# Optimization experiments

Hardware: AMD Instinct MI355X
Metric: run time of the kernel (lower is better)

## Reference

```python
import jax, jax.numpy as jnp
import numpy as np

N = 20000      # nodes
E = 320000     # edges (before self-loops)
C_IN, C_HID, C_OUT = 256, 256, 128
NEG_SLOPE = 0.2  # PyG GATConv default


def setup_inputs() -> dict:
    key = jax.random.key(0)
    ks = jax.random.split(key, 10)
    x = jax.random.normal(ks[0], (N, C_IN), dtype=jnp.float32)
    edge_index = jax.random.randint(ks[1], (2, E), 0, N, dtype=jnp.int64)

    def glorot(k, shape, fan):
        return jax.random.normal(k, shape, dtype=jnp.float32) / np.float32(np.sqrt(fan))

    W1 = glorot(ks[2], (C_IN, C_HID), C_IN)
    a_src1 = glorot(ks[3], (C_HID,), C_HID)
    a_dst1 = glorot(ks[4], (C_HID,), C_HID)
    b1 = jnp.zeros((C_HID,), jnp.float32)
    W2 = glorot(ks[5], (C_HID, C_OUT), C_HID)
    a_src2 = glorot(ks[6], (C_OUT,), C_OUT)
    a_dst2 = glorot(ks[7], (C_OUT,), C_OUT)
    b2 = jnp.zeros((C_OUT,), jnp.float32)
    return dict(x=x, edge_index=edge_index, W1=W1, a_src1=a_src1, a_dst1=a_dst1,
                b1=b1, W2=W2, a_src2=a_src2, a_dst2=a_dst2, b2=b2)


def gat_layer(x, src, dst, W, a_src, a_dst, b, n):
    # PyG GATConv (heads=1): linear proj, additive attention, softmax over
    # incoming edges per destination node, weighted aggregation + bias.
    h = x @ W                                   # [N, F]
    alpha_src = h @ a_src                       # [N]
    alpha_dst = h @ a_dst                       # [N]
    e = jax.nn.leaky_relu(alpha_src[src] + alpha_dst[dst], NEG_SLOPE)  # [E]
    m = jax.ops.segment_max(e, dst, num_segments=n)                    # stable softmax
    e = jnp.exp(e - m[dst])
    denom = jax.ops.segment_sum(e, dst, num_segments=n)                # [N]
    out = jax.ops.segment_sum(e[:, None] * h[src], dst, num_segments=n)  # [N, F]
    return out / denom[:, None] + b


def reference(x, edge_index, W1, a_src1, a_dst1, b1, W2, a_src2, a_dst2, b2):
    n = x.shape[0]
    # GATConv adds self-loops by default
    loops = jnp.arange(n, dtype=edge_index.dtype)
    ei = jnp.concatenate([edge_index, jnp.stack([loops, loops])], axis=1)
    src, dst = ei[0], ei[1]
    h = gat_layer(x, src, dst, W1, a_src1, a_dst1, b1, n)
    h = jax.nn.relu(h)  # Dropout is identity in eval mode
    return gat_layer(h, src, dst, W2, a_src2, a_dst2, b2, n)
```

## Files before the change

### kernel.cpp

```cpp
#include <hip/hip_runtime.h>
#include <math.h>

#define N_NODES 20000
#define N_EDGES 320000
#define E_TOT   (N_EDGES + N_NODES)
#define C_IN  256
#define C_HID 256
#define C_OUT 128
#define NEG_SLOPE 0.2f
#define CAP   256

typedef __attribute__((ext_vector_type(8))) short bf16x8;
typedef __attribute__((ext_vector_type(4))) float f32x4;

__device__ __align__(16) unsigned short c_W1h[C_IN * C_HID], c_W1l[C_IN * C_HID];
__device__ __align__(16) unsigned short c_W2h[C_HID * C_OUT], c_W2l[C_HID * C_OUT];
__device__ float c_as1f[C_HID], c_ad1f[C_HID], c_b1f[C_HID];
__device__ float c_as2f[C_OUT], c_ad2f[C_OUT], c_b2f[C_OUT];
__device__ __align__(16) unsigned short g_h1b[(size_t)N_NODES * C_HID];
__device__ __align__(16) unsigned short g_g1h[(size_t)N_NODES * C_HID];
__device__ __align__(16) unsigned short g_g1l[(size_t)N_NODES * C_HID];
__device__ __align__(16) unsigned short g_h2b[(size_t)N_NODES * C_OUT];
__device__ float g_alps1[N_NODES], g_alpd1[N_NODES];
__device__ float g_alps2[N_NODES], g_alpd2[N_NODES];
__device__ int   g_cursor[N_NODES];
__device__ int   g_srcidx[(size_t)N_NODES * CAP];
__device__ int   g_is64;
__device__ int   g_isf32;

__device__ __forceinline__ float bf2f(unsigned short b){
  unsigned int u = ((unsigned int)b) << 16;
  return __builtin_bit_cast(float, u);
}
__device__ __forceinline__ unsigned short f2bf(float f){
  unsigned int u = __builtin_bit_cast(unsigned int, f);
  u += 0x7fffu + ((u >> 16) & 1u);
  return (unsigned short)(u >> 16);
}
__device__ __forceinline__ int clampi(int v){
  v = v < 0 ? 0 : v;
  return v >= N_NODES ? N_NODES - 1 : v;
}
__device__ __forceinline__ void edge_sd(const int* ei, int e, int& s, int& d){
  if (e < N_EDGES){
    if (g_is64){ s = ei[2 * e]; d = ei[2 * (N_EDGES + e)]; }
    else       { s = ei[e];     d = ei[N_EDGES + e]; }
    s = clampi(s); d = clampi(d);
  } else {
    s = d = e - N_EDGES;
  }
}

struct Ptrs { const void* p[8]; };

__device__ __forceinline__ int wpack(int k, int n, int Nc){
  return (((k >> 5) * (Nc / 16) + (n >> 4)) * 64 + (((k >> 3) & 3) * 16 + (n & 15))) * 8 + (k & 7);
}

#define PREP_Z  N_NODES
#define PREP_W1 (C_IN * C_HID)
#define PREP_W2 (C_HID * C_OUT)
#define PREP_T  (PREP_Z + PREP_W1 + PREP_W2 + 2 * C_HID + C_HID + 2 * C_OUT + C_OUT)

__global__ void prep_k(const unsigned int* __restrict__ xw,
                       const int* __restrict__ ei, Ptrs ps){
  __shared__ int s_isf32;
  if (threadIdx.x < 64){
    int lane = (int)threadIdx.x, cnt = 0;
    for (int j = lane; j < 256; j += 64){
      unsigned int e = (xw[j] >> 7) & 0xFFu;
      if (e >= 0x60u && e <= 0x8Fu) ++cnt;
    }
#pragma unroll
    for (int o = 32; o > 0; o >>= 1) cnt += __shfl_xor(cnt, o, 64);
    if (lane == 0) s_isf32 = (cnt < 200) ? 1 : 0;
  }
  __syncthreads();
  const int isf32 = s_isf32;

  if (blockIdx.x == 0 && threadIdx.x < 64){
    unsigned long long anybad = __ballot(ei[2 * (int)threadIdx.x + 1] != 0);
    if (threadIdx.x == 0){ g_isf32 = isf32; g_is64 = (anybad == 0ULL) ? 1 : 0; }
  }

  int tid = (int)(blockIdx.x * blockDim.x + threadIdx.x);
  if (tid < PREP_Z){
    g_cursor[tid] = 0;
    g_alps1[tid] = 0.f; g_alpd1[tid] = 0.f;
    g_alps2[tid] = 0.f; g_alpd2[tid] = 0.f;
    return;
  }
  int j = tid - PREP_Z;
  auto ld = [&](const void* p, int i) -> float {
    return isf32 ? ((const float*)p)[i] : bf2f(((const unsigned short*)p)[i]);
  };
  if (j < PREP_W1){
    float f = ld(ps.p[0], j);
    int k = j / C_HID, n = j % C_HID;
    int idx = wpack(k, n, C_HID);
    unsigned short h = f2bf(f);
    c_W1h[idx] = h; c_W1l[idx] = f2bf(f - bf2f(h));
    return;
  }
  j -= PREP_W1;
  if (j < PREP_W2){
    float f = ld(ps.p[4], j);
    int k = j / C_OUT, n = j % C_OUT;
    int idx = wpack(k, n, C_OUT);
    unsigned short h = f2bf(f);
    c_W2h[idx] = h; c_W2l[idx] = f2bf(f - bf2f(h));
    return;
  }
  j -= PREP_W2;
  if      (j <  256) c_as1f[j]        = ld(ps.p[1], j);
  else if (j <  512) c_ad1f[j - 256]  = ld(ps.p[2], j - 256);
  else if (j <  768) c_b1f [j - 512]  = ld(ps.p[3], j - 512);
  else if (j <  896) c_as2f[j - 768]  = ld(ps.p[5], j - 768);
  else if (j < 1024) c_ad2f[j - 896]  = ld(ps.p[6], j - 896);
  else if (j < 1152) c_b2f [j - 1024] = ld(ps.p[7], j - 1024);
}

__global__ void scatter_k(const int* __restrict__ ei){
  int e = blockIdx.x * blockDim.x + threadIdx.x;
  if (e >= E_TOT) return;
  int s, d;
  edge_sd(ei, e, s, d);
  int pos = atomicAdd(&g_cursor[d], 1);
  if (pos < CAP) g_srcidx[(size_t)d * CAP + pos] = s;
}

template<int SEL>
__global__ __launch_bounds__(256) void gemm_k(const void* __restrict__ xsrc){
  const int Nc = SEL ? C_OUT : C_HID;
  const int NT = SEL ? 2 : 4;
  const unsigned short* Wh = SEL ? c_W2h : c_W1h;
  const unsigned short* Wl = SEL ? c_W2l : c_W1l;
  unsigned short* Hb = SEL ? g_h2b : g_h1b;
  float* alps = SEL ? g_alps2 : g_alps1;
  float* alpd = SEL ? g_alpd2 : g_alpd1;
  const float* aS = SEL ? c_as2f : c_as1f;
  const float* aD = SEL ? c_ad2f : c_ad1f;
  const bool isf32 = (SEL == 0) && (g_isf32 != 0);

  int wave = (int)(threadIdx.x >> 6);
  int lane = (int)(threadIdx.x & 63);
  int kgrp = lane >> 4, cl = lane & 15;
  int mbase = blockIdx.x * 32;

  f32x4 acc[2][4];
#pragma unroll
  for (int m = 0; m < 2; ++m)
#pragma unroll
    for (int n = 0; n < NT; ++n) acc[m][n] = (f32x4){0.f, 0.f, 0.f, 0.f};

  for (int kt = 0; kt < 8; ++kt){
    int kbase = kt * 32 + kgrp * 8;
    bf16x8 ah[2], al[2];
    if (SEL == 1){
#pragma unroll
      for (int m = 0; m < 2; ++m){
        size_t ai = (size_t)(mbase + m * 16 + cl) * 256 + kbase;
        ah[m] = *(const bf16x8*)(g_g1h + ai);
        al[m] = *(const bf16x8*)(g_g1l + ai);
      }
    } else if (isf32){
      const float* Xf = (const float*)xsrc;
#pragma unroll
      for (int m = 0; m < 2; ++m){
        const float4* xp = (const float4*)(Xf + (size_t)(mbase + m * 16 + cl) * 256 + kbase);
        float4 v0 = xp[0], v1 = xp[1];
        float vals[8] = {v0.x, v0.y, v0.z, v0.w, v1.x, v1.y, v1.z, v1.w};
#pragma unroll
        for (int j = 0; j < 8; ++j){
          unsigned short h = f2bf(vals[j]);
          ah[m][j] = (short)h;
          al[m][j] = (short)f2bf(vals[j] - bf2f(h));
        }
      }
    } else {
      const unsigned short* Xb = (const unsigned short*)xsrc;
#pragma unroll
      for (int m = 0; m < 2; ++m){
        ah[m] = *(const bf16x8*)(Xb + (size_t)(mbase + m * 16 + cl) * 256 + kbase);
        al[m] = (bf16x8){0,0,0,0,0,0,0,0};
      }
    }
#pragma unroll
    for (int nn = 0; nn < NT; ++nn){
      int nt = wave * NT + nn;
      size_t wi = ((size_t)(kt * (Nc / 16) + nt) * 64 + lane) * 8;
      bf16x8 bh = *(const bf16x8*)(Wh + wi);
      bf16x8 bl = *(const bf16x8*)(Wl + wi);
#pragma unroll
      for (int m = 0; m < 2; ++m){
        acc[m][nn] = __builtin_amdgcn_mfma_f32_16x16x32_bf16(ah[m], bh, acc[m][nn], 0, 0, 0);
        acc[m][nn] = __builtin_amdgcn_mfma_f32_16x16x32_bf16(ah[m], bl, acc[m][nn], 0, 0, 0);
        acc[m][nn] = __builtin_amdgcn_mfma_f32_16x16x32_bf16(al[m], bh, acc[m][nn], 0, 0, 0);
      }
    }
  }

  float asv[4], adv[4];
#pragma unroll
  for (int nn = 0; nn < NT; ++nn){
    int col = (wave * NT + nn) * 16 + cl;
    asv[nn] = aS[col]; adv[nn] = aD[col];
  }
#pragma unroll
  for (int m = 0; m < 2; ++m){
#pragma unroll
    for (int i = 0; i < 4; ++i){
      int row = mbase + m * 16 + kgrp * 4 + i;
      float ps = 0.f, pd = 0.f;
#pragma unroll
      for (int nn = 0; nn < NT; ++nn){
        int col = (wave * NT + nn) * 16 + cl;
        float v = acc[m][nn][i];
        Hb[(size_t)row * Nc + col] = f2bf(v);
        ps += v * asv[nn]; pd += v * adv[nn];
      }
      ps += __shfl_xor(ps, 1);  pd += __shfl_xor(pd, 1);
      ps += __shfl_xor(ps, 2);  pd += __shfl_xor(pd, 2);
      ps += __shfl_xor(ps, 4);  pd += __shfl_xor(pd, 4);
      ps += __shfl_xor(ps, 8);  pd += __shfl_xor(pd, 8);
      if (cl == 0){
        atomicAdd(&alps[row], ps);
        atomicAdd(&alpd[row], pd);
      }
    }
  }
}

#define ACC4(p, ww) { \
  a0 += (ww) * bf2f((unsigned short)((p).x & 0xFFFFu)); \
  a1 += (ww) * bf2f((unsigned short)((p).x >> 16)); \
  a2 += (ww) * bf2f((unsigned short)((p).y & 0xFFFFu)); \
  a3 += (ww) * bf2f((unsigned short)((p).y >> 16)); }

#define ACC2(p, ww) { \
  a0 += (ww) * bf2f((unsigned short)((p) & 0xFFFFu)); \
  a1 += (ww) * bf2f((unsigned short)((p) >> 16)); }

template<int F, int SEL>
__global__ void agg_k(float* OUT){
  const unsigned short* Hb = SEL ? g_h2b : g_h1b;
  const float* bias = SEL ? c_b2f : c_b1f;
  const float* alps = SEL ? g_alps2 : g_alps1;
  const float* alpd = SEL ? g_alpd2 : g_alpd1;
  int lane = threadIdx.x & 63;
  int n = blockIdx.x * 4 + (threadIdx.x >> 6);
  int len = g_cursor[n]; if (len > CAP) len = CAP;
  int i0 = n * CAP, i1 = i0 + len;
  float adn = alpd[n];
  float dpart = 0.f;
  float a0 = 0.f, a1 = 0.f, a2 = 0.f, a3 = 0.f;
  const uint2* H2 = (const uint2*)Hb;
  const unsigned int* H1 = (const unsigned int*)Hb;

  for (int base = i0; base < i1; base += 64){
    int nv = i1 - base; if (nv > 64) nv = 64;
    int sv = 0; float wv = 0.f;
    if (lane < nv){
      sv = g_srcidx[base + lane];
      float e = alps[sv] + adn;
      e = (e > 0.f) ? e : NEG_SLOPE * e;
      wv = __expf(e);
    }
    dpart += wv;
    int j = 0;
    for (; j + 8 <= nv; j += 8){
      int s0 = __shfl(sv, j),     s1 = __shfl(sv, j + 1);
      int s2 = __shfl(sv, j + 2), s3 = __shfl(sv, j + 3);
      int s4 = __shfl(sv, j + 4), s5 = __shfl(sv, j + 5);
      int s6 = __shfl(sv, j + 6), s7 = __shfl(sv, j + 7);
      float w0 = __shfl(wv, j),     w1 = __shfl(wv, j + 1);
      float w2 = __shfl(wv, j + 2), w3 = __shfl(wv, j + 3);
      float w4 = __shfl(wv, j + 4), w5 = __shfl(wv, j + 5);
      float w6 = __shfl(wv, j + 6), w7 = __shfl(wv, j + 7);
      if constexpr (F == 256){
        uint2 p0 = H2[(size_t)s0 * 64 + lane];
        uint2 p1 = H2[(size_t)s1 * 64 + lane];
        uint2 p2 = H2[(size_t)s2 * 64 + lane];
        uint2 p3 = H2[(size_t)s3 * 64 + lane];
        uint2 p4 = H2[(size_t)s4 * 64 + lane];
        uint2 p5 = H2[(size_t)s5 * 64 + lane];
        uint2 p6 = H2[(size_t)s6 * 64 + lane];
        uint2 p7 = H2[(size_t)s7 * 64 + lane];
        ACC4(p0, w0) ACC4(p1, w1) ACC4(p2, w2) ACC4(p3, w3)
        ACC4(p4, w4) ACC4(p5, w5) ACC4(p6, w6) ACC4(p7, w7)
      } else {
        unsigned int p0 = H1[(size_t)s0 * 64 + lane];
        unsigned int p1 = H1[(size_t)s1 * 64 + lane];
        unsigned int p2 = H1[(size_t)s2 * 64 + lane];
        unsigned int p3 = H1[(size_t)s3 * 64 + lane];
        unsigned int p4 = H1[(size_t)s4 * 64 + lane];
        unsigned int p5 = H1[(size_t)s5 * 64 + lane];
        unsigned int p6 = H1[(size_t)s6 * 64 + lane];
        unsigned int p7 = H1[(size_t)s7 * 64 + lane];
        ACC2(p0, w0) ACC2(p1, w1) ACC2(p2, w2) ACC2(p3, w3)
        ACC2(p4, w4) ACC2(p5, w5) ACC2(p6, w6) ACC2(p7, w7)
      }
    }
    for (; j + 4 <= nv; j += 4){
      int s0 = __shfl(sv, j),     s1 = __shfl(sv, j + 1);
      int s2 = __shfl(sv, j + 2), s3 = __shfl(sv, j + 3);
      float w0 = __shfl(wv, j),     w1 = __shfl(wv, j + 1);
      float w2 = __shfl(wv, j + 2), w3 = __shfl(wv, j + 3);
      if constexpr (F == 256){
        uint2 p0 = H2[(size_t)s0 * 64 + lane];
        uint2 p1 = H2[(size_t)s1 * 64 + lane];
        uint2 p2 = H2[(size_t)s2 * 64 + lane];
        uint2 p3 = H2[(size_t)s3 * 64 + lane];
        ACC4(p0, w0) ACC4(p1, w1) ACC4(p2, w2) ACC4(p3, w3)
      } else {
        unsigned int p0 = H1[(size_t)s0 * 64 + lane];
        unsigned int p1 = H1[(size_t)s1 * 64 + lane];
        unsigned int p2 = H1[(size_t)s2 * 64 + lane];
        unsigned int p3 = H1[(size_t)s3 * 64 + lane];
        ACC2(p0, w0) ACC2(p1, w1) ACC2(p2, w2) ACC2(p3, w3)
      }
    }
    for (; j < nv; ++j){
      int s = __shfl(sv, j);
      float w = __shfl(wv, j);
      if constexpr (F == 256){
        uint2 p = H2[(size_t)s * 64 + lane];
        ACC4(p, w)
      } else {
        unsigned int p = H1[(size_t)s * 64 + lane];
        ACC2(p, w)
      }
    }
  }

  float den = dpart;
#pragma unroll
  for (int o = 32; o > 0; o >>= 1) den += __shfl_xor(den, o, 64);
  float inv = 1.f / den;

  if constexpr (F == 256){
    float o0 = a0 * inv + bias[4 * lane];
    float o1 = a1 * inv + bias[4 * lane + 1];
    float o2 = a2 * inv + bias[4 * lane + 2];
    float o3 = a3 * inv + bias[4 * lane + 3];
    if (SEL == 0){
      o0 = fmaxf(o0, 0.f); o1 = fmaxf(o1, 0.f);
      o2 = fmaxf(o2, 0.f); o3 = fmaxf(o3, 0.f);
      unsigned short h0 = f2bf(o0), h1 = f2bf(o1), h2 = f2bf(o2), h3 = f2bf(o3);
      uint2 ph, pl;
      ph.x = (unsigned)h0 | ((unsigned)h1 << 16);
      ph.y = (unsigned)h2 | ((unsigned)h3 << 16);
      pl.x = (unsigned)f2bf(o0 - bf2f(h0)) | ((unsigned)f2bf(o1 - bf2f(h1)) << 16);
      pl.y = (unsigned)f2bf(o2 - bf2f(h2)) | ((unsigned)f2bf(o3 - bf2f(h3)) << 16);
      ((uint2*)g_g1h)[(size_t)n * 64 + lane] = ph;
      ((uint2*)g_g1l)[(size_t)n * 64 + lane] = pl;
    } else {
      float4 o; o.x = o0; o.y = o1; o.z = o2; o.w = o3;
      ((float4*)OUT)[(size_t)n * 64 + lane] = o;
    }
  } else {
    float o0 = a0 * inv + bias[2 * lane];
    float o1 = a1 * inv + bias[2 * lane + 1];
    if (SEL == 0){
      o0 = fmaxf(o0, 0.f); o1 = fmaxf(o1, 0.f);
      unsigned short h0 = f2bf(o0), h1 = f2bf(o1);
      ((unsigned int*)g_g1h)[(size_t)n * 64 + lane] = (unsigned)h0 | ((unsigned)h1 << 16);
      ((unsigned int*)g_g1l)[(size_t)n * 64 + lane] =
        (unsigned)f2bf(o0 - bf2f(h0)) | ((unsigned)f2bf(o1 - bf2f(h1)) << 16);
    } else {
      float2 o; o.x = o0; o.y = o1;
      ((float2*)OUT)[(size_t)n * 64 + lane] = o;
    }
  }
}

extern "C" void kernel_launch(void* const* d_in, const int* in_sizes, int n_in,
                              void* d_out, int out_size, void* d_ws, size_t ws_size,
                              hipStream_t stream){
  (void)in_sizes; (void)n_in; (void)out_size; (void)d_ws; (void)ws_size;
  const void* x  = d_in[0];
  const int*  ei = (const int*)d_in[1];
  float* out = (float*)d_out;

  Ptrs ps;
  ps.p[0] = d_in[2]; ps.p[1] = d_in[3]; ps.p[2] = d_in[4]; ps.p[3] = d_in[5];
  ps.p[4] = d_in[6]; ps.p[5] = d_in[7]; ps.p[6] = d_in[8]; ps.p[7] = d_in[9];

  prep_k<<<(PREP_T + 255) / 256, 256, 0, stream>>>((const unsigned int*)x, ei, ps);
  scatter_k<<<(E_TOT + 255) / 256, 256, 0, stream>>>(ei);

  gemm_k<0><<<N_NODES / 32, 256, 0, stream>>>(x);
  agg_k<C_HID, 0><<<N_NODES / 4, 256, 0, stream>>>(nullptr);

  gemm_k<1><<<N_NODES / 32, 256, 0, stream>>>(nullptr);
  agg_k<C_OUT, 1><<<N_NODES / 4, 256, 0, stream>>>(out);
}
```

Baseline: 192.5 us.

## Split each node's edge list across two wavefronts and handle self-loops inline

```diff
diff --git a/kernel.cpp b/kernel.cpp
--- a/kernel.cpp
+++ b/kernel.cpp
@@ -3,7 +3,6 @@
 
 #define N_NODES 20000
 #define N_EDGES 320000
-#define E_TOT   (N_EDGES + N_NODES)
 #define C_IN  256
 #define C_HID 256
 #define C_OUT 128
@@ -42,13 +41,9 @@
   return v >= N_NODES ? N_NODES - 1 : v;
 }
 __device__ __forceinline__ void edge_sd(const int* ei, int e, int& s, int& d){
-  if (e < N_EDGES){
-    if (g_is64){ s = ei[2 * e]; d = ei[2 * (N_EDGES + e)]; }
-    else       { s = ei[e];     d = ei[N_EDGES + e]; }
-    s = clampi(s); d = clampi(d);
-  } else {
-    s = d = e - N_EDGES;
-  }
+  if (g_is64){ s = ei[2 * e]; d = ei[2 * (N_EDGES + e)]; }
+  else       { s = ei[e];     d = ei[N_EDGES + e]; }
+  s = clampi(s); d = clampi(d);
 }
 
 struct Ptrs { const void* p[8]; };
@@ -122,7 +117,7 @@
 
 __global__ void scatter_k(const int* __restrict__ ei){
   int e = blockIdx.x * blockDim.x + threadIdx.x;
-  if (e >= E_TOT) return;
+  if (e >= N_EDGES) return;
   int s, d;
   edge_sd(ei, e, s, d);
   int pos = atomicAdd(&g_cursor[d], 1);
@@ -242,41 +237,63 @@
   a1 += (ww) * bf2f((unsigned short)((p) >> 16)); }
 
 template<int F, int SEL>
-__global__ void agg_k(float* OUT){
+__global__ __launch_bounds__(256) void agg_k(float* OUT){
   const unsigned short* Hb = SEL ? g_h2b : g_h1b;
   const float* bias = SEL ? c_b2f : c_b1f;
   const float* alps = SEL ? g_alps2 : g_alps1;
   const float* alpd = SEL ? g_alpd2 : g_alpd1;
+  __shared__ float lds_a[4][64][4];
+  __shared__ float lds_d[4][64];
+
   int lane = threadIdx.x & 63;
-  int n = blockIdx.x * 4 + (threadIdx.x >> 6);
+  int wv   = (int)(threadIdx.x >> 6);
+  int half = wv & 1;
+  int n = blockIdx.x * 2 + (wv >> 1);
+
   int len = g_cursor[n]; if (len > CAP) len = CAP;
-  int i0 = n * CAP, i1 = i0 + len;
+  int lenA = len >> 1;
+  int i0 = n * CAP + (half ? lenA : 0);
+  int i1 = n * CAP + (half ? len : lenA);
   float adn = alpd[n];
   float dpart = 0.f;
   float a0 = 0.f, a1 = 0.f, a2 = 0.f, a3 = 0.f;
   const uint2* H2 = (const uint2*)Hb;
   const unsigned int* H1 = (const unsigned int*)Hb;
 
+  if (half == 0){
+    float es = alps[n] + adn;
+    es = (es > 0.f) ? es : NEG_SLOPE * es;
+    float wself = __expf(es);
+    if (lane == 0) dpart += wself;
+    if constexpr (F == 256){
+      uint2 p = H2[(size_t)n * 64 + lane];
+      ACC4(p, wself)
+    } else {
+      unsigned int p = H1[(size_t)n * 64 + lane];
+      ACC2(p, wself)
+    }
+  }
+
   for (int base = i0; base < i1; base += 64){
     int nv = i1 - base; if (nv > 64) nv = 64;
-    int sv = 0; float wv = 0.f;
+    int sv = 0; float wvv = 0.f;
     if (lane < nv){
       sv = g_srcidx[base + lane];
       float e = alps[sv] + adn;
       e = (e > 0.f) ? e : NEG_SLOPE * e;
-      wv = __expf(e);
-    }
-    dpart += wv;
+      wvv = __expf(e);
+    }
+    dpart += wvv;
     int j = 0;
     for (; j + 8 <= nv; j += 8){
       int s0 = __shfl(sv, j),     s1 = __shfl(sv, j + 1);
       int s2 = __shfl(sv, j + 2), s3 = __shfl(sv, j + 3);
       int s4 = __shfl(sv, j + 4), s5 = __shfl(sv, j + 5);
       int s6 = __shfl(sv, j + 6), s7 = __shfl(sv, j + 7);
-      float w0 = __shfl(wv, j),     w1 = __shfl(wv, j + 1);
-      float w2 = __shfl(wv, j + 2), w3 = __shfl(wv, j + 3);
-      float w4 = __shfl(wv, j + 4), w5 = __shfl(wv, j + 5);
-      float w6 = __shfl(wv, j + 6), w7 = __shfl(wv, j + 7);
+      float w0 = __shfl(wvv, j),     w1 = __shfl(wvv, j + 1);
+      float w2 = __shfl(wvv, j + 2), w3 = __shfl(wvv, j + 3);
+      float w4 = __shfl(wvv, j + 4), w5 = __shfl(wvv, j + 5);
+      float w6 = __shfl(wvv, j + 6), w7 = __shfl(wvv, j + 7);
       if constexpr (F == 256){
         uint2 p0 = H2[(size_t)s0 * 64 + lane];
         uint2 p1 = H2[(size_t)s1 * 64 + lane];
@@ -304,8 +321,8 @@
     for (; j + 4 <= nv; j += 4){
       int s0 = __shfl(sv, j),     s1 = __shfl(sv, j + 1);
       int s2 = __shfl(sv, j + 2), s3 = __shfl(sv, j + 3);
-      float w0 = __shfl(wv, j),     w1 = __shfl(wv, j + 1);
-      float w2 = __shfl(wv, j + 2), w3 = __shfl(wv, j + 3);
+      float w0 = __shfl(wvv, j),     w1 = __shfl(wvv, j + 1);
+      float w2 = __shfl(wvv, j + 2), w3 = __shfl(wvv, j + 3);
       if constexpr (F == 256){
         uint2 p0 = H2[(size_t)s0 * 64 + lane];
         uint2 p1 = H2[(size_t)s1 * 64 + lane];
@@ -322,7 +339,7 @@
     }
     for (; j < nv; ++j){
       int s = __shfl(sv, j);
-      float w = __shfl(wv, j);
+      float w = __shfl(wvv, j);
       if constexpr (F == 256){
         uint2 p = H2[(size_t)s * 64 + lane];
         ACC4(p, w)
@@ -333,7 +350,14 @@
     }
   }
 
-  float den = dpart;
+  lds_a[wv][lane][0] = a0; lds_a[wv][lane][1] = a1;
+  lds_a[wv][lane][2] = a2; lds_a[wv][lane][3] = a3;
+  lds_d[wv][lane] = dpart;
+  __syncthreads();
+  if (half) return;
+  a0 += lds_a[wv + 1][lane][0]; a1 += lds_a[wv + 1][lane][1];
+  a2 += lds_a[wv + 1][lane][2]; a3 += lds_a[wv + 1][lane][3];
+  float den = dpart + lds_d[wv + 1][lane];
 #pragma unroll
   for (int o = 32; o > 0; o >>= 1) den += __shfl_xor(den, o, 64);
   float inv = 1.f / den;
@@ -387,11 +411,11 @@
   ps.p[4] = d_in[6]; ps.p[5] = d_in[7]; ps.p[6] = d_in[8]; ps.p[7] = d_in[9];
 
   prep_k<<<(PREP_T + 255) / 256, 256, 0, stream>>>((const unsigned int*)x, ei, ps);
-  scatter_k<<<(E_TOT + 255) / 256, 256, 0, stream>>>(ei);
+  scatter_k<<<(N_EDGES + 255) / 256, 256, 0, stream>>>(ei);
 
   gemm_k<0><<<N_NODES / 32, 256, 0, stream>>>(x);
-  agg_k<C_HID, 0><<<N_NODES / 4, 256, 0, stream>>>(nullptr);
+  agg_k<C_HID, 0><<<N_NODES / 2, 256, 0, stream>>>(nullptr);
 
   gemm_k<1><<<N_NODES / 32, 256, 0, stream>>>(nullptr);
-  agg_k<C_OUT, 1><<<N_NODES / 4, 256, 0, stream>>>(out);
-}
+  agg_k<C_OUT, 1><<<N_NODES / 2, 256, 0, stream>>>(out);
+}
```

Result: no change. 195.7 us (+1.7%).

## Fuse edge scatter into first GEMM launch and handle self-loops in aggregation

Applied to the files above, without the earlier changes.

```diff
diff --git a/kernel.cpp b/kernel.cpp
--- a/kernel.cpp
+++ b/kernel.cpp
@@ -3,12 +3,13 @@
 
 #define N_NODES 20000
 #define N_EDGES 320000
-#define E_TOT   (N_EDGES + N_NODES)
 #define C_IN  256
 #define C_HID 256
 #define C_OUT 128
 #define NEG_SLOPE 0.2f
 #define CAP   256
+#define GEMM1_BLKS (N_NODES / 32)
+#define SCAT_BLKS  ((N_EDGES + 255) / 256)
 
 typedef __attribute__((ext_vector_type(8))) short bf16x8;
 typedef __attribute__((ext_vector_type(4))) float f32x4;
@@ -42,13 +43,9 @@
   return v >= N_NODES ? N_NODES - 1 : v;
 }
 __device__ __forceinline__ void edge_sd(const int* ei, int e, int& s, int& d){
-  if (e < N_EDGES){
-    if (g_is64){ s = ei[2 * e]; d = ei[2 * (N_EDGES + e)]; }
-    else       { s = ei[e];     d = ei[N_EDGES + e]; }
-    s = clampi(s); d = clampi(d);
-  } else {
-    s = d = e - N_EDGES;
-  }
+  if (g_is64){ s = ei[2 * e]; d = ei[2 * (N_EDGES + e)]; }
+  else       { s = ei[e];     d = ei[N_EDGES + e]; }
+  s = clampi(s); d = clampi(d);
 }
 
 struct Ptrs { const void* p[8]; };
@@ -120,17 +117,20 @@
   else if (j < 1152) c_b2f [j - 1024] = ld(ps.p[7], j - 1024);
 }
 
-__global__ void scatter_k(const int* __restrict__ ei){
-  int e = blockIdx.x * blockDim.x + threadIdx.x;
-  if (e >= E_TOT) return;
-  int s, d;
-  edge_sd(ei, e, s, d);
-  int pos = atomicAdd(&g_cursor[d], 1);
-  if (pos < CAP) g_srcidx[(size_t)d * CAP + pos] = s;
-}
-
 template<int SEL>
-__global__ __launch_bounds__(256) void gemm_k(const void* __restrict__ xsrc){
+__global__ __launch_bounds__(256) void gemm_k(const void* __restrict__ xsrc,
+                                              const int* __restrict__ ei){
+  if (SEL == 0 && blockIdx.x >= GEMM1_BLKS){
+    int e = (int)(blockIdx.x - GEMM1_BLKS) * 256 + (int)threadIdx.x;
+    if (e < N_EDGES){
+      int s, d;
+      edge_sd(ei, e, s, d);
+      int pos = atomicAdd(&g_cursor[d], 1);
+      if (pos < CAP) g_srcidx[(size_t)d * CAP + pos] = s;
+    }
+    return;
+  }
+
   const int Nc = SEL ? C_OUT : C_HID;
   const int NT = SEL ? 2 : 4;
   const unsigned short* Wh = SEL ? c_W2h : c_W1h;
@@ -256,6 +256,20 @@
   float a0 = 0.f, a1 = 0.f, a2 = 0.f, a3 = 0.f;
   const uint2* H2 = (const uint2*)Hb;
   const unsigned int* H1 = (const unsigned int*)Hb;
+
+  {
+    float es = alps[n] + adn;
+    es = (es > 0.f) ? es : NEG_SLOPE * es;
+    float wself = __expf(es);
+    if (lane == 0) dpart += wself;
+    if constexpr (F == 256){
+      uint2 p = H2[(size_t)n * 64 + lane];
+      ACC4(p, wself)
+    } else {
+      unsigned int p = H1[(size_t)n * 64 + lane];
+      ACC2(p, wself)
+    }
+  }
 
   for (int base = i0; base < i1; base += 64){
     int nv = i1 - base; if (nv > 64) nv = 64;
@@ -387,11 +401,10 @@
   ps.p[4] = d_in[6]; ps.p[5] = d_in[7]; ps.p[6] = d_in[8]; ps.p[7] = d_in[9];
 
   prep_k<<<(PREP_T + 255) / 256, 256, 0, stream>>>((const unsigned int*)x, ei, ps);
-  scatter_k<<<(E_TOT + 255) / 256, 256, 0, stream>>>(ei);
-
-  gemm_k<0><<<N_NODES / 32, 256, 0, stream>>>(x);
+
+  gemm_k<0><<<GEMM1_BLKS + SCAT_BLKS, 256, 0, stream>>>(x, ei);
   agg_k<C_HID, 0><<<N_NODES / 4, 256, 0, stream>>>(nullptr);
 
-  gemm_k<1><<<N_NODES / 32, 256, 0, stream>>>(nullptr);
+  gemm_k<1><<<N_NODES / 32, 256, 0, stream>>>(nullptr, nullptr);
   agg_k<C_OUT, 1><<<N_NODES / 4, 256, 0, stream>>>(out);
 }
```

Measured after the change: 184.0 us. 1.05x faster.
